# Kernel optimization log

Measured on AMD Instinct MI355X. Metric: run time of the kernel, lower is better.

The kernel has to match this reference:

```python
import jax, jax.numpy as jnp
import numpy as np


def _relu(x):
    return jnp.maximum(x, 0)


def _conv(x, w, b):
    # x: [M, Cin, H, W], w: [Cout, Cin, 3, 3], VALID padding, stride 1, ReLU
    y = jax.lax.conv_general_dilated(x, w, (1, 1), 'VALID',
                                     dimension_numbers=('NCHW', 'OIHW', 'NCHW'))
    return _relu(y + b[None, :, None, None])


def setup_inputs() -> dict:
    key = jax.random.key(0)
    ks = jax.random.split(key, 16)
    B, N, C, H, W = 32, 64, 16, 30, 30
    E, A = 128, 5
    s = 0.05
    f32 = jnp.float32
    states = jax.random.normal(ks[0], (B, N, C, H, W), f32)
    adjacencies = jax.random.uniform(ks[1], (B, N, N), f32)
    inactives = jax.random.randint(ks[2], (B, N), 0, 2).astype(bool)
    # conv block: C -> 16 -> 32 -> 16 -> 16, 3x3 VALID
    cw0 = jax.random.normal(ks[3], (16, C, 3, 3), f32) * s; cb0 = jnp.zeros((16,), f32)
    cw1 = jax.random.normal(ks[4], (32, 16, 3, 3), f32) * s; cb1 = jnp.zeros((32,), f32)
    cw2 = jax.random.normal(ks[5], (16, 32, 3, 3), f32) * s; cb2 = jnp.zeros((16,), f32)
    cw3 = jax.random.normal(ks[6], (16, 16, 3, 3), f32) * s; cb3 = jnp.zeros((16,), f32)
    flat = 16 * (H - 8) * (W - 8)  # 16*22*22 = 7744
    # encoder MLP: flat -> 128 -> 128 -> E
    mw0 = jax.random.normal(ks[7], (flat, 128), f32) * s; mb0 = jnp.zeros((128,), f32)
    mw1 = jax.random.normal(ks[8], (128, 128), f32) * s; mb1 = jnp.zeros((128,), f32)
    mw2 = jax.random.normal(ks[9], (128, E), f32) * s; mb2 = jnp.zeros((E,), f32)
    # GCNConv: E -> E
    gw = jax.random.normal(ks[10], (E, E), f32) * s; gb = jnp.zeros((E,), f32)
    # DQN head: E -> 128 -> 128 -> A
    fw0 = jax.random.normal(ks[11], (E, 128), f32) * s; fb0 = jnp.zeros((128,), f32)
    fw1 = jax.random.normal(ks[12], (128, 128), f32) * s; fb1 = jnp.zeros((128,), f32)
    fw2 = jax.random.normal(ks[13], (128, A), f32) * s; fb2 = jnp.zeros((A,), f32)
    return dict(states=states, adjacencies=adjacencies, inactives=inactives,
                cw0=cw0, cb0=cb0, cw1=cw1, cb1=cb1, cw2=cw2, cb2=cb2, cw3=cw3, cb3=cb3,
                mw0=mw0, mb0=mb0, mw1=mw1, mb1=mb1, mw2=mw2, mb2=mb2,
                gw=gw, gb=gb, fw0=fw0, fb0=fb0, fw1=fw1, fb1=fb1, fw2=fw2, fb2=fb2)


def reference(states, adjacencies, inactives,
              cw0, cb0, cw1, cb1, cw2, cb2, cw3, cb3,
              mw0, mb0, mw1, mb1, mw2, mb2,
              gw, gb, fw0, fb0, fw1, fb1, fw2, fb2):
    B, N = states.shape[0], states.shape[1]
    # per-agent CNN encoder, batched over all (batch, agent) pairs
    x = states.reshape((B * N,) + states.shape[2:])
    for w, b in ((cw0, cb0), (cw1, cb1), (cw2, cb2), (cw3, cb3)):
        x = _conv(x, w, b)
    x = x.reshape(B * N, -1)
    x = _relu(x @ mw0 + mb0)
    x = _relu(x @ mw1 + mb1)
    feats = (x @ mw2 + mb2).reshape(B, N, -1)  # [B, N, E]
    # GCNConv with symmetric normalization (add_self_loops=False; the original
    # edge-list loop is equivalent to dense propagation with A as edge weights)
    deg = adjacencies.sum(axis=1)  # deg[b, j] = sum_i A[b, i, j] (target degree)
    dis = jnp.where(deg > 0, jax.lax.rsqrt(jnp.maximum(deg, 1e-30)), 0.0)
    h = feats @ gw  # [B, N, E]
    norm = dis[:, :, None] * adjacencies * dis[:, None, :]  # norm[b, i, j]
    emb = jnp.einsum('bij,bid->bjd', norm, h) + gb  # messages i -> j
    # per-agent DQN head; inactive agents keep zero q-values
    q = _relu(emb @ fw0 + fb0)
    q = _relu(q @ fw1 + fb1)
    q = q @ fw2 + fb2  # [B, N, action_size]
    return jnp.where(inactives[..., None], 0.0, q)
```

## Files before the change

### kernel.cpp

```cpp
#include <hip/hip_runtime.h>


__global__ void k_mask(const void* __restrict__ raw, int* __restrict__ mask)
{
    __shared__ unsigned pat[8];
    __shared__ int layout;
    const unsigned char* bts = (const unsigned char*)raw;
    const unsigned* w = (const unsigned*)raw;
    const unsigned short* hw = (const unsigned short*)raw;
    const int t = threadIdx.x;
    if (t < 8) pat[t] = 0;
    __syncthreads();
    unsigned loc[8] = {0,0,0,0,0,0,0,0};
    for (int i = t * 8; i < 2048; i += 256 * 8)
#pragma unroll
        for (int r = 0; r < 8; ++r) loc[r] |= bts[i + r];
#pragma unroll
    for (int r = 0; r < 8; ++r) if (loc[r]) atomicOr(&pat[r], loc[r]);
    __syncthreads();
    if (t == 0) {
        int L = 0;
        bool smallOnly = true;
#pragma unroll
        for (int r = 0; r < 8; ++r) smallOnly = smallOnly && (pat[r] <= 1u);
        if (smallOnly) {
            if (pat[1] | pat[2] | pat[3] | pat[5] | pat[6] | pat[7]) L = 1;
            else if (pat[4] == 0 && pat[0])                          L = 2;
            else                                                     L = 0;
        } else {
            if (pat[1] | pat[5])      L = 4;
            else if (pat[2] | pat[6]) L = 3;
            else if (pat[7])          L = 5;
        }
        layout = L;
    }
    __syncthreads();
    const int L = layout;
    for (int m = t; m < 2048; m += 256) {
        unsigned v;
        if      (L == 1) v = bts[m];
        else if (L == 2) v = w[2 * m] | w[2 * m + 1];
        else if (L == 3) v = w[m];
        else if (L == 4) v = hw[m];
        else if (L == 5) v = w[2 * m] | w[2 * m + 1];
        else             v = w[m];
        mask[m] = (v != 0u);
    }
}

template<int OW>
__device__ __forceinline__ void row_sweep(
    const float* __restrict__ r0, const float* __restrict__ r1,
    const float* __restrict__ r2,
    const float* __restrict__ w0, const float* __restrict__ w1,
    float* __restrict__ acc0, float* __restrict__ acc1)
{
    float a[3][8] __attribute__((aligned(16)));
    *(float4*)&a[0][0] = *(const float4*)r0;
    *(float4*)&a[1][0] = *(const float4*)r1;
    *(float4*)&a[2][0] = *(const float4*)r2;
#pragma unroll
    for (int cx = 0; cx < OW; cx += 4) {
        if (OW - cx > 2) {
            *(float4*)&a[0][4] = *(const float4*)(r0 + cx + 4);
            *(float4*)&a[1][4] = *(const float4*)(r1 + cx + 4);
            *(float4*)&a[2][4] = *(const float4*)(r2 + cx + 4);
        }
#pragma unroll
        for (int j = 0; j < 4; ++j) {
            if (cx + j < OW) {
#pragma unroll
                for (int ky = 0; ky < 3; ++ky)
#pragma unroll
                    for (int kx = 0; kx < 3; ++kx) {
                        acc0[cx + j] = fmaf(w0[ky * 3 + kx], a[ky][j + kx], acc0[cx + j]);
                        acc1[cx + j] = fmaf(w1[ky * 3 + kx], a[ky][j + kx], acc1[cx + j]);
                    }
            }
        }
#pragma unroll
        for (int ky = 0; ky < 3; ++ky)
            *(float4*)&a[ky][0] = *(float4*)&a[ky][4];
    }
}

__global__ __launch_bounds__(256, 2)
void k_convA(const float* __restrict__ st,
             const float* __restrict__ cw0, const float* __restrict__ cb0,
             const float* __restrict__ cw1, const float* __restrict__ cb1,
             float* __restrict__ y1)
{
    __shared__ float sY0[16 * 784];
    __shared__ float sIn[2 * 1080];
    __shared__ float sW[2 * 384];
    const int t = threadIdx.x;
    const int bId = blockIdx.x;
    const float* stb = st + (size_t)bId * 14400;

    const int g0 = t >> 5;
    const int row0 = t & 31;
    const bool act0 = row0 < 28;

    float acc[2][28];
#pragma unroll
    for (int o = 0; o < 2; ++o)
#pragma unroll
        for (int c = 0; c < 28; ++c) acc[o][c] = 0.f;

    auto stage_in0 = [&](int ic, int buf) {
        if (t < 225) {
            float4 v = *(const float4*)&stb[ic * 900 + t * 4];
            float vv[4] = {v.x, v.y, v.z, v.w};
            int e = t * 4;
#pragma unroll
            for (int k = 0; k < 4; ++k) {
                int ee = e + k;
                sIn[buf * 1080 + (ee / 30) * 36 + (ee % 30)] = vv[k];
            }
        }
    };
    auto stage_w0 = [&](int ic, int buf) {
        if (t < 192) {
            int oc = t / 12, k = t % 12;
            if (k < 9) sW[buf * 384 + t] = cw0[(oc * 16 + ic) * 9 + k];
        }
    };

    stage_in0(0, 0); stage_w0(0, 0);
#pragma unroll 1
    for (int ic = 0; ic < 16; ++ic) {
        __syncthreads();
        if (ic + 1 < 16) { stage_in0(ic + 1, (ic + 1) & 1); stage_w0(ic + 1, (ic + 1) & 1); }
        if (act0) {
            const int buf = ic & 1;
            float w0r[12] __attribute__((aligned(16)));
            float w1r[12] __attribute__((aligned(16)));
#pragma unroll
            for (int q = 0; q < 3; ++q) {
                *(float4*)&w0r[q * 4] = *(const float4*)&sW[buf * 384 + (2 * g0 + 0) * 12 + q * 4];
                *(float4*)&w1r[q * 4] = *(const float4*)&sW[buf * 384 + (2 * g0 + 1) * 12 + q * 4];
            }
            const float* b = &sIn[buf * 1080 + row0 * 36];
            row_sweep<28>(b, b + 36, b + 72, w0r, w1r, acc[0], acc[1]);
        }
    }
    if (act0) {
#pragma unroll
        for (int o = 0; o < 2; ++o) {
            float bv = cb0[2 * g0 + o];
            float* dst = &sY0[(2 * g0 + o) * 784 + row0 * 28];
#pragma unroll
            for (int cx = 0; cx < 28; cx += 4) {
                float4 v;
                v.x = fmaxf(acc[o][cx + 0] + bv, 0.f);
                v.y = fmaxf(acc[o][cx + 1] + bv, 0.f);
                v.z = fmaxf(acc[o][cx + 2] + bv, 0.f);
                v.w = fmaxf(acc[o][cx + 3] + bv, 0.f);
                *(float4*)&dst[cx] = v;
            }
        }
    }
    __syncthreads();

    auto stage_w1 = [&](int ic, int buf) {
        for (int e = t; e < 384; e += 256) {
            int oc = e / 12, k = e % 12;
            if (k < 9) sW[buf * 384 + e] = cw1[(oc * 16 + ic) * 9 + k];
        }
    };
    stage_w1(0, 0);
    const int g1 = t >> 4;
    const int l1 = t & 15;
#pragma unroll 1
    for (int p = 0; p < 2; ++p) {
        const int row = l1 + 16 * p;
        const bool act1 = row < 26;
        float a1[2][26];
#pragma unroll
        for (int o = 0; o < 2; ++o)
#pragma unroll
            for (int c = 0; c < 26; ++c) a1[o][c] = 0.f;
#pragma unroll 1
        for (int ic = 0; ic < 16; ++ic) {
            __syncthreads();
            int s = p * 16 + ic;
            if (s + 1 < 32) stage_w1((s + 1) & 15, (s + 1) & 1);
            if (act1) {
                const int buf = s & 1;
                float w0r[12] __attribute__((aligned(16)));
                float w1r[12] __attribute__((aligned(16)));
#pragma unroll
                for (int q = 0; q < 3; ++q) {
                    *(float4*)&w0r[q * 4] = *(const float4*)&sW[buf * 384 + (2 * g1 + 0) * 12 + q * 4];
                    *(float4*)&w1r[q * 4] = *(const float4*)&sW[buf * 384 + (2 * g1 + 1) * 12 + q * 4];
                }
                const float* b = &sY0[ic * 784 + row * 28];
                row_sweep<26>(b, b + 28, b + 56, w0r, w1r, a1[0], a1[1]);
            }
        }
        if (act1) {
#pragma unroll
            for (int o = 0; o < 2; ++o) {
                float bv = cb1[2 * g1 + o];
                float* dst = &y1[((size_t)bId * 32 + (2 * g1 + o)) * 676 + row * 26];
#pragma unroll
                for (int cx = 0; cx < 26; cx += 2) {
                    float2 v;
                    v.x = fmaxf(a1[o][cx + 0] + bv, 0.f);
                    v.y = fmaxf(a1[o][cx + 1] + bv, 0.f);
                    *(float2*)&dst[cx] = v;
                }
            }
        }
    }
}

__global__ __launch_bounds__(256, 3)
void k_convB(const float* __restrict__ y1,
             const float* __restrict__ cw2, const float* __restrict__ cb2,
             const float* __restrict__ cw3, const float* __restrict__ cb3,
             float* __restrict__ y3)
{
    __shared__ float sY2[16 * 672];
    __shared__ float sIn[2 * 768];
    __shared__ float sW[2 * 192];
    const int t = threadIdx.x;
    const int bId = blockIdx.x;
    const int g = t >> 5;
    const int row = t & 31;

    const bool act2 = row < 24;
    float acc[2][24];
#pragma unroll
    for (int o = 0; o < 2; ++o)
#pragma unroll
        for (int c = 0; c < 24; ++c) acc[o][c] = 0.f;

    auto stage_in2 = [&](int ic, int buf) {
        if (t < 169) {
            float4 v = *(const float4*)&y1[((size_t)bId * 32 + ic) * 676 + t * 4];
            float vv[4] = {v.x, v.y, v.z, v.w};
            int e = t * 4;
#pragma unroll
            for (int k = 0; k < 4; ++k) {
                int ee = e + k;
                sIn[buf * 768 + (ee / 26) * 28 + (ee % 26)] = vv[k];
            }
        }
    };
    auto stage_w2 = [&](int ic, int buf) {
        if (t < 192) {
            int oc = t / 12, k = t % 12;
            if (k < 9) sW[buf * 192 + t] = cw2[(oc * 32 + ic) * 9 + k];
        }
    };

    stage_in2(0, 0); stage_w2(0, 0);
#pragma unroll 1
    for (int ic = 0; ic < 32; ++ic) {
        __syncthreads();
        if (ic + 1 < 32) { stage_in2(ic + 1, (ic + 1) & 1); stage_w2(ic + 1, (ic + 1) & 1); }
        if (act2) {
            const int buf = ic & 1;
            float w0r[12] __attribute__((aligned(16)));
            float w1r[12] __attribute__((aligned(16)));
#pragma unroll
            for (int q = 0; q < 3; ++q) {
                *(float4*)&w0r[q * 4] = *(const float4*)&sW[buf * 192 + (2 * g + 0) * 12 + q * 4];
                *(float4*)&w1r[q * 4] = *(const float4*)&sW[buf * 192 + (2 * g + 1) * 12 + q * 4];
            }
            const float* b = &sIn[buf * 768 + row * 28];
            row_sweep<24>(b, b + 28, b + 56, w0r, w1r, acc[0], acc[1]);
        }
    }
    if (act2) {
#pragma unroll
        for (int o = 0; o < 2; ++o) {
            float bv = cb2[2 * g + o];
            float* dst = &sY2[(2 * g + o) * 672 + row * 28];
#pragma unroll
            for (int cx = 0; cx < 24; cx += 4) {
                float4 v;
                v.x = fmaxf(acc[o][cx + 0] + bv, 0.f);
                v.y = fmaxf(acc[o][cx + 1] + bv, 0.f);
                v.z = fmaxf(acc[o][cx + 2] + bv, 0.f);
                v.w = fmaxf(acc[o][cx + 3] + bv, 0.f);
                *(float4*)&dst[cx] = v;
            }
        }
    }
    __syncthreads();

    auto stage_w3 = [&](int ic, int buf) {
        if (t < 192) {
            int oc = t / 12, k = t % 12;
            if (k < 9) sW[buf * 192 + t] = cw3[(oc * 16 + ic) * 9 + k];
        }
    };
    stage_w3(0, 0);
    const bool act3 = row < 22;
    float a3[2][22];
#pragma unroll
    for (int o = 0; o < 2; ++o)
#pragma unroll
        for (int c = 0; c < 22; ++c) a3[o][c] = 0.f;
#pragma unroll 1
    for (int ic = 0; ic < 16; ++ic) {
        __syncthreads();
        if (ic + 1 < 16) stage_w3(ic + 1, (ic + 1) & 1);
        if (act3) {
            const int buf = ic & 1;
            float w0r[12] __attribute__((aligned(16)));
            float w1r[12] __attribute__((aligned(16)));
#pragma unroll
            for (int q = 0; q < 3; ++q) {
                *(float4*)&w0r[q * 4] = *(const float4*)&sW[buf * 192 + (2 * g + 0) * 12 + q * 4];
                *(float4*)&w1r[q * 4] = *(const float4*)&sW[buf * 192 + (2 * g + 1) * 12 + q * 4];
            }
            const float* b = &sY2[ic * 672 + row * 28];
            row_sweep<22>(b, b + 28, b + 56, w0r, w1r, a3[0], a3[1]);
        }
    }
    if (act3) {
#pragma unroll
        for (int o = 0; o < 2; ++o) {
            float bv = cb3[2 * g + o];
            float* dst = &y3[(size_t)bId * 7744 + (2 * g + o) * 484 + row * 22];
#pragma unroll
            for (int cx = 0; cx < 22; cx += 2) {
                float2 v;
                v.x = fmaxf(a3[o][cx + 0] + bv, 0.f);
                v.y = fmaxf(a3[o][cx + 1] + bv, 0.f);
                *(float2*)&dst[cx] = v;
            }
        }
    }
}

__global__ __launch_bounds__(256)
void k_mlp0(const float* __restrict__ y3, const float* __restrict__ mw0,
            float* __restrict__ part)
{
    __shared__ float As[8 * 32];
    __shared__ float Bs[8 * 128];
    const int t  = threadIdx.x;
    const int mt = blockIdx.x;
    const int ks = blockIdx.y;
    const int m0g = mt * 32;
    const int kb0 = ks * 968;
    const int tm = t >> 4, tn = t & 15;
    const int m0 = tm * 2, n0 = tn * 8;
    float acc[2][8];
#pragma unroll
    for (int r = 0; r < 2; ++r)
#pragma unroll
        for (int c = 0; c < 8; ++c) acc[r][c] = 0.f;

    for (int it = 0; it < 121; ++it) {
        const int kb = kb0 + it * 8;
        if (t < 64) {
            int m = t >> 1, q = t & 1;
            const float4 a4 = *(const float4*)&y3[(m0g + m) * 7744 + kb + q * 4];
            As[(q * 4 + 0) * 32 + m] = a4.x;
            As[(q * 4 + 1) * 32 + m] = a4.y;
            As[(q * 4 + 2) * 32 + m] = a4.z;
            As[(q * 4 + 3) * 32 + m] = a4.w;
        }
        {
            int kk = t >> 5, n4 = t & 31;
            *(float4*)&Bs[kk * 128 + n4 * 4] = *(const float4*)&mw0[(kb + kk) * 128 + n4 * 4];
        }
        __syncthreads();
#pragma unroll
        for (int kk = 0; kk < 8; ++kk) {
            float a0 = As[kk * 32 + m0];
            float a1 = As[kk * 32 + m0 + 1];
            float4 b0 = *(const float4*)&Bs[kk * 128 + n0];
            float4 b1 = *(const float4*)&Bs[kk * 128 + n0 + 4];
            float br[8] = {b0.x, b0.y, b0.z, b0.w, b1.x, b1.y, b1.z, b1.w};
#pragma unroll
            for (int c = 0; c < 8; ++c) {
                acc[0][c] = fmaf(a0, br[c], acc[0][c]);
                acc[1][c] = fmaf(a1, br[c], acc[1][c]);
            }
        }
        __syncthreads();
    }
#pragma unroll
    for (int r = 0; r < 2; ++r)
#pragma unroll
        for (int c = 0; c < 8; ++c)
            part[ks * 262144 + (m0g + m0 + r) * 128 + n0 + c] = acc[r][c];
}

__global__ void k_red(const float* __restrict__ part, const float* __restrict__ mb0,
                      float* __restrict__ z0)
{
    int idx = blockIdx.x * 256 + threadIdx.x;
    int n = idx & 127;
    float s = mb0[n];
#pragma unroll
    for (int k = 0; k < 8; ++k) s += part[k * 262144 + idx];
    z0[idx] = fmaxf(s, 0.f);
}

__global__ __launch_bounds__(256)
void k_fc(const float* __restrict__ A, const float* __restrict__ W,
          const float* __restrict__ bias, float* __restrict__ C, int do_relu)
{
    __shared__ float As[32 * 129];
    __shared__ float Ws[32 * 128];
    const int t = threadIdx.x;
    const int m0g = blockIdx.x * 32;
#pragma unroll
    for (int r = 0; r < 16; ++r) {
        int e = t + r * 256; int m = e >> 7, k = e & 127;
        As[m * 129 + k] = A[(m0g + m) * 128 + k];
    }
    const int tm = t >> 4, tn = t & 15;
    const int m0 = tm * 2, n0 = tn * 8;
    float acc[2][8];
#pragma unroll
    for (int r = 0; r < 2; ++r)
#pragma unroll
        for (int c = 0; c < 8; ++c) acc[r][c] = 0.f;

    for (int kc = 0; kc < 4; ++kc) {
        __syncthreads();
#pragma unroll
        for (int r = 0; r < 16; ++r) {
            int e = t + r * 256; int kk = e >> 7, n = e & 127;
            Ws[kk * 128 + n] = W[(kc * 32 + kk) * 128 + n];
        }
        __syncthreads();
#pragma unroll
        for (int kk = 0; kk < 32; ++kk) {
            float a0 = As[(m0 + 0) * 129 + kc * 32 + kk];
            float a1 = As[(m0 + 1) * 129 + kc * 32 + kk];
            float4 b0 = *(const float4*)&Ws[kk * 128 + n0];
            float4 b1 = *(const float4*)&Ws[kk * 128 + n0 + 4];
            float br[8] = {b0.x, b0.y, b0.z, b0.w, b1.x, b1.y, b1.z, b1.w};
#pragma unroll
            for (int c = 0; c < 8; ++c) {
                acc[0][c] = fmaf(a0, br[c], acc[0][c]);
                acc[1][c] = fmaf(a1, br[c], acc[1][c]);
            }
        }
    }
#pragma unroll
    for (int c = 0; c < 8; ++c) {
        float bv = bias ? bias[n0 + c] : 0.f;
#pragma unroll
        for (int r = 0; r < 2; ++r) {
            float v = acc[r][c] + bv;
            if (do_relu) v = fmaxf(v, 0.f);
            C[(m0g + m0 + r) * 128 + n0 + c] = v;
        }
    }
}

__global__ void k_dis(const float* __restrict__ adj, float* __restrict__ dis)
{
    int bj = blockIdx.x * 256 + threadIdx.x;
    int b = bj >> 6, j = bj & 63;
    float s = 0.f;
#pragma unroll 4
    for (int i = 0; i < 64; ++i) s += adj[b * 4096 + i * 64 + j];
    dis[bj] = s > 0.f ? rsqrtf(fmaxf(s, 1e-30f)) : 0.f;
}

__global__ __launch_bounds__(256)
void k_gcn(const float* __restrict__ adj, const float* __restrict__ dis,
           const float* __restrict__ h, const float* __restrict__ gb,
           float* __restrict__ emb)
{
    __shared__ float adjn[64 * 64];
    __shared__ float hS[64 * 128];
    __shared__ float disS[64];
    const int t = threadIdx.x;
    const int b = blockIdx.x;
    if (t < 64) disS[t] = dis[b * 64 + t];
    __syncthreads();
#pragma unroll
    for (int r = 0; r < 16; ++r) {
        int e = t + r * 256; int i = e >> 6;
        adjn[e] = adj[b * 4096 + e] * disS[i];
    }
#pragma unroll
    for (int r = 0; r < 32; ++r) {
        int e = t + r * 256;
        hS[e] = h[b * 8192 + e];
    }
    __syncthreads();
    const int tj = t >> 5, tn = t & 31;
    const int j0 = tj * 8, n0 = tn * 4;
    float acc[8][4];
#pragma unroll
    for (int jj = 0; jj < 8; ++jj)
#pragma unroll
        for (int c = 0; c < 4; ++c) acc[jj][c] = 0.f;
    for (int i = 0; i < 64; ++i) {
        float4 h4 = *(const float4*)&hS[i * 128 + n0];
        float hr[4] = {h4.x, h4.y, h4.z, h4.w};
#pragma unroll
        for (int jj = 0; jj < 8; ++jj) {
            float a = adjn[i * 64 + j0 + jj];
#pragma unroll
            for (int c = 0; c < 4; ++c) acc[jj][c] = fmaf(a, hr[c], acc[jj][c]);
        }
    }
#pragma unroll
    for (int jj = 0; jj < 8; ++jj) {
        float dj = disS[j0 + jj];
#pragma unroll
        for (int c = 0; c < 4; ++c)
            emb[b * 8192 + (j0 + jj) * 128 + n0 + c] = dj * acc[jj][c] + gb[n0 + c];
    }
}

__global__ __launch_bounds__(256)
void k_head(const float* __restrict__ q1, const float* __restrict__ fw2,
            const float* __restrict__ fb2, const int* __restrict__ maskN,
            float* __restrict__ out)
{
    __shared__ float qs[256 * 33];
    __shared__ float w2s[640];
    __shared__ float b2s[5];
    const int t = threadIdx.x;
    const int m0g = blockIdx.x * 256;
    if (t < 5) b2s[t] = fb2[t];
#pragma unroll
    for (int r = 0; r < 3; ++r) {
        int e = t + r * 256;
        if (e < 640) w2s[e] = fw2[e];
    }
    float acc[5] = {0.f, 0.f, 0.f, 0.f, 0.f};
    for (int kc = 0; kc < 4; ++kc) {
        __syncthreads();
#pragma unroll
        for (int r = 0; r < 32; ++r) {
            int e = t + r * 256; int m = e >> 5, k = e & 31;
            qs[m * 33 + k] = q1[(m0g + m) * 128 + kc * 32 + k];
        }
        __syncthreads();
#pragma unroll
        for (int k = 0; k < 32; ++k) {
            float v = qs[t * 33 + k];
#pragma unroll
            for (int a = 0; a < 5; ++a) acc[a] = fmaf(v, w2s[(kc * 32 + k) * 5 + a], acc[a]);
        }
    }
    const int m = m0g + t;
    const int iz = maskN[m];
#pragma unroll
    for (int a = 0; a < 5; ++a) out[m * 5 + a] = iz ? 0.f : (acc[a] + b2s[a]);
}

extern "C" void kernel_launch(void* const* d_in, const int* in_sizes, int n_in,
                              void* d_out, int out_size, void* d_ws, size_t ws_size,
                              hipStream_t stream)
{
    (void)in_sizes; (void)n_in; (void)out_size;
    const float* states = (const float*)d_in[0];
    const float* adj    = (const float*)d_in[1];
    const void*  inact  = (const void*) d_in[2];
    const float* cw0 = (const float*)d_in[3];  const float* cb0 = (const float*)d_in[4];
    const float* cw1 = (const float*)d_in[5];  const float* cb1 = (const float*)d_in[6];
    const float* cw2 = (const float*)d_in[7];  const float* cb2 = (const float*)d_in[8];
    const float* cw3 = (const float*)d_in[9];  const float* cb3 = (const float*)d_in[10];
    const float* mw0 = (const float*)d_in[11]; const float* mb0 = (const float*)d_in[12];
    const float* mw1 = (const float*)d_in[13]; const float* mb1 = (const float*)d_in[14];
    const float* mw2 = (const float*)d_in[15]; const float* mb2 = (const float*)d_in[16];
    const float* gw  = (const float*)d_in[17]; const float* gb  = (const float*)d_in[18];
    const float* fw0 = (const float*)d_in[19]; const float* fb0 = (const float*)d_in[20];
    const float* fw1 = (const float*)d_in[21]; const float* fb1 = (const float*)d_in[22];
    const float* fw2 = (const float*)d_in[23]; const float* fb2 = (const float*)d_in[24];
    float* out = (float*)d_out;

    const size_t HDR_FL = 4096, Y3_FL = 15859712, TAIL_FL = 3932160;
    const size_t Y1_PER_IMG = 21632;
    size_t ws_fl = ws_size / 4;
    int nsplit = 32;
    for (int n = 1; n <= 32; n *= 2) {
        size_t imgs = (2048 + (size_t)n - 1) / n;
        size_t y1fl = imgs * Y1_PER_IMG;
        size_t need = HDR_FL + Y3_FL + (y1fl > TAIL_FL ? y1fl : TAIL_FL);
        if (need <= ws_fl) { nsplit = n; break; }
    }

    float* ws    = (float*)d_ws;
    int*   maskN = (int*)ws;
    float* dis   = ws + 2048;
    float* y3    = ws + HDR_FL;
    float* dyn   = y3 + Y3_FL;
    float* y1g   = dyn;
    float* part  = dyn;
    float* z0    = part + 2097152;
    float* z1    = z0   + 262144;
    float* feats = z1   + 262144;
    float* h     = feats + 262144;
    float* emb   = h    + 262144;
    float* q0    = emb  + 262144;
    float* q1    = q0   + 262144;

    k_mask<<<1, 256, 0, stream>>>(inact, maskN);

    const int per = (2048 + nsplit - 1) / nsplit;
    for (int s = 0; s < nsplit; ++s) {
        int i0 = s * per;
        int cnt = 2048 - i0; if (cnt > per) cnt = per;
        if (cnt <= 0) break;
        k_convA<<<cnt, 256, 0, stream>>>(states + (size_t)i0 * 14400,
                                         cw0, cb0, cw1, cb1, y1g);
        k_convB<<<cnt, 256, 0, stream>>>(y1g, cw2, cb2, cw3, cb3,
                                         y3 + (size_t)i0 * 7744);
    }

    k_mlp0<<<dim3(64, 8), 256, 0, stream>>>(y3, mw0, part);
    k_red<<<1024, 256, 0, stream>>>(part, mb0, z0);
    k_fc<<<64, 256, 0, stream>>>(z0, mw1, mb1, z1, 1);
    k_fc<<<64, 256, 0, stream>>>(z1, mw2, mb2, feats, 0);
    k_fc<<<64, 256, 0, stream>>>(feats, gw, nullptr, h, 0);
    k_dis<<<8, 256, 0, stream>>>(adj, dis);
    k_gcn<<<32, 256, 0, stream>>>(adj, dis, h, gb, emb);
    k_fc<<<64, 256, 0, stream>>>(emb, fw0, fb0, q0, 1);
    k_fc<<<64, 256, 0, stream>>>(q0, fw1, fb1, q1, 1);
    k_head<<<8, 256, 0, stream>>>(q1, fw2, fb2, maskN, out);
}
```

Measured before the change: 1.033 ms.

## Preload conv weights into shared memory once and enlarge mlp0 tile

The conv kernels now stage each layer's full weight set into shared memory once, in an arena that reuses the input staging buffers. This removes per-input-channel weight staging and most barriers in the conv1 and conv3 loops. The first MLP GEMM tile grows from 32 to 64 rows per block, with a 4x8 register tile per thread and split column groups, so each weight tile is reused across more rows. Shared memory grows and the mlp0 grid halves, which may reduce occupancy or parallelism.

```diff
diff --git a/kernel.cpp b/kernel.cpp
--- a/kernel.cpp
+++ b/kernel.cpp
@@ -90,12 +90,22 @@
              const float* __restrict__ cw1, const float* __restrict__ cb1,
              float* __restrict__ y1)
 {
-    __shared__ float sY0[16 * 784];
-    __shared__ float sIn[2 * 1080];
-    __shared__ float sW[2 * 384];
+    __shared__ float arena[12544 + 6272];
+    float* const sY0 = arena;
+    float* const regB = arena + 12544;
+    float* const sIn = regB;
+    float* const sW0 = regB + 2160;
+    float* const sW1 = regB;
+
     const int t = threadIdx.x;
     const int bId = blockIdx.x;
     const float* stb = st + (size_t)bId * 14400;
+
+    {
+#pragma unroll
+        for (int k = 0; k < 9; ++k)
+            sW0[(t >> 4) * 196 + (t & 15) * 12 + k] = cw0[t * 9 + k];
+    }
 
     const int g0 = t >> 5;
     const int row0 = t & 31;
@@ -119,26 +129,20 @@
             }
         }
     };
-    auto stage_w0 = [&](int ic, int buf) {
-        if (t < 192) {
-            int oc = t / 12, k = t % 12;
-            if (k < 9) sW[buf * 384 + t] = cw0[(oc * 16 + ic) * 9 + k];
-        }
-    };
-
-    stage_in0(0, 0); stage_w0(0, 0);
+
+    stage_in0(0, 0);
 #pragma unroll 1
     for (int ic = 0; ic < 16; ++ic) {
         __syncthreads();
-        if (ic + 1 < 16) { stage_in0(ic + 1, (ic + 1) & 1); stage_w0(ic + 1, (ic + 1) & 1); }
+        if (ic + 1 < 16) stage_in0(ic + 1, (ic + 1) & 1);
         if (act0) {
             const int buf = ic & 1;
             float w0r[12] __attribute__((aligned(16)));
             float w1r[12] __attribute__((aligned(16)));
 #pragma unroll
             for (int q = 0; q < 3; ++q) {
-                *(float4*)&w0r[q * 4] = *(const float4*)&sW[buf * 384 + (2 * g0 + 0) * 12 + q * 4];
-                *(float4*)&w1r[q * 4] = *(const float4*)&sW[buf * 384 + (2 * g0 + 1) * 12 + q * 4];
+                *(float4*)&w0r[q * 4] = *(const float4*)&sW0[(2 * g0 + 0) * 196 + ic * 12 + q * 4];
+                *(float4*)&w1r[q * 4] = *(const float4*)&sW0[(2 * g0 + 1) * 196 + ic * 12 + q * 4];
             }
             const float* b = &sIn[buf * 1080 + row0 * 36];
             row_sweep<28>(b, b + 36, b + 72, w0r, w1r, acc[0], acc[1]);
@@ -162,13 +166,14 @@
     }
     __syncthreads();
 
-    auto stage_w1 = [&](int ic, int buf) {
-        for (int e = t; e < 384; e += 256) {
-            int oc = e / 12, k = e % 12;
-            if (k < 9) sW[buf * 384 + e] = cw1[(oc * 16 + ic) * 9 + k];
-        }
-    };
-    stage_w1(0, 0);
+    for (int e = t; e < 512; e += 256) {
+        int oc = e >> 4, ic = e & 15;
+#pragma unroll
+        for (int k = 0; k < 9; ++k)
+            sW1[oc * 196 + ic * 12 + k] = cw1[e * 9 + k];
+    }
+    __syncthreads();
+
     const int g1 = t >> 4;
     const int l1 = t & 15;
 #pragma unroll 1
@@ -180,25 +185,19 @@
         for (int o = 0; o < 2; ++o)
 #pragma unroll
             for (int c = 0; c < 26; ++c) a1[o][c] = 0.f;
+        if (act1) {
 #pragma unroll 1
-        for (int ic = 0; ic < 16; ++ic) {
-            __syncthreads();
-            int s = p * 16 + ic;
-            if (s + 1 < 32) stage_w1((s + 1) & 15, (s + 1) & 1);
-            if (act1) {
-                const int buf = s & 1;
+            for (int ic = 0; ic < 16; ++ic) {
                 float w0r[12] __attribute__((aligned(16)));
                 float w1r[12] __attribute__((aligned(16)));
 #pragma unroll
                 for (int q = 0; q < 3; ++q) {
-                    *(float4*)&w0r[q * 4] = *(const float4*)&sW[buf * 384 + (2 * g1 + 0) * 12 + q * 4];
-                    *(float4*)&w1r[q * 4] = *(const float4*)&sW[buf * 384 + (2 * g1 + 1) * 12 + q * 4];
+                    *(float4*)&w0r[q * 4] = *(const float4*)&sW1[(2 * g1 + 0) * 196 + ic * 12 + q * 4];
+                    *(float4*)&w1r[q * 4] = *(const float4*)&sW1[(2 * g1 + 1) * 196 + ic * 12 + q * 4];
                 }
                 const float* b = &sY0[ic * 784 + row * 28];
                 row_sweep<26>(b, b + 28, b + 56, w0r, w1r, a1[0], a1[1]);
             }
-        }
-        if (act1) {
 #pragma unroll
             for (int o = 0; o < 2; ++o) {
                 float bv = cb1[2 * g1 + o];
@@ -221,9 +220,13 @@
              const float* __restrict__ cw3, const float* __restrict__ cb3,
              float* __restrict__ y3)
 {
-    __shared__ float sY2[16 * 672];
-    __shared__ float sIn[2 * 768];
-    __shared__ float sW[2 * 192];
+    __shared__ float arena2[10752 + 2304];
+    float* const sY2 = arena2;
+    float* const regB = arena2 + 10752;
+    float* const sIn = regB;
+    float* const sW2 = regB + 1536;
+    float* const sW3 = regB;
+
     const int t = threadIdx.x;
     const int bId = blockIdx.x;
     const int g = t >> 5;
@@ -251,7 +254,7 @@
     auto stage_w2 = [&](int ic, int buf) {
         if (t < 192) {
             int oc = t / 12, k = t % 12;
-            if (k < 9) sW[buf * 192 + t] = cw2[(oc * 32 + ic) * 9 + k];
+            if (k < 9) sW2[buf * 192 + t] = cw2[(oc * 32 + ic) * 9 + k];
         }
     };
 
@@ -266,8 +269,8 @@
             float w1r[12] __attribute__((aligned(16)));
 #pragma unroll
             for (int q = 0; q < 3; ++q) {
-                *(float4*)&w0r[q * 4] = *(const float4*)&sW[buf * 192 + (2 * g + 0) * 12 + q * 4];
-                *(float4*)&w1r[q * 4] = *(const float4*)&sW[buf * 192 + (2 * g + 1) * 12 + q * 4];
+                *(float4*)&w0r[q * 4] = *(const float4*)&sW2[buf * 192 + (2 * g + 0) * 12 + q * 4];
+                *(float4*)&w1r[q * 4] = *(const float4*)&sW2[buf * 192 + (2 * g + 1) * 12 + q * 4];
             }
             const float* b = &sIn[buf * 768 + row * 28];
             row_sweep<24>(b, b + 28, b + 56, w0r, w1r, acc[0], acc[1]);
@@ -291,37 +294,27 @@
     }
     __syncthreads();
 
-    auto stage_w3 = [&](int ic, int buf) {
-        if (t < 192) {
-            int oc = t / 12, k = t % 12;
-            if (k < 9) sW[buf * 192 + t] = cw3[(oc * 16 + ic) * 9 + k];
-        }
-    };
-    stage_w3(0, 0);
+    for (int e = t; e < 2304; e += 256) sW3[e] = cw3[e];
+    __syncthreads();
+
     const bool act3 = row < 22;
     float a3[2][22];
 #pragma unroll
     for (int o = 0; o < 2; ++o)
 #pragma unroll
         for (int c = 0; c < 22; ++c) a3[o][c] = 0.f;
+    if (act3) {
 #pragma unroll 1
-    for (int ic = 0; ic < 16; ++ic) {
-        __syncthreads();
-        if (ic + 1 < 16) stage_w3(ic + 1, (ic + 1) & 1);
-        if (act3) {
-            const int buf = ic & 1;
-            float w0r[12] __attribute__((aligned(16)));
-            float w1r[12] __attribute__((aligned(16)));
-#pragma unroll
-            for (int q = 0; q < 3; ++q) {
-                *(float4*)&w0r[q * 4] = *(const float4*)&sW[buf * 192 + (2 * g + 0) * 12 + q * 4];
-                *(float4*)&w1r[q * 4] = *(const float4*)&sW[buf * 192 + (2 * g + 1) * 12 + q * 4];
+        for (int ic = 0; ic < 16; ++ic) {
+            float w0r[9], w1r[9];
+#pragma unroll
+            for (int k = 0; k < 9; ++k) {
+                w0r[k] = sW3[((2 * g + 0) * 16 + ic) * 9 + k];
+                w1r[k] = sW3[((2 * g + 1) * 16 + ic) * 9 + k];
             }
             const float* b = &sY2[ic * 672 + row * 28];
             row_sweep<22>(b, b + 28, b + 56, w0r, w1r, a3[0], a3[1]);
         }
-    }
-    if (act3) {
 #pragma unroll
         for (int o = 0; o < 2; ++o) {
             float bv = cb3[2 * g + o];
@@ -341,30 +334,30 @@
 void k_mlp0(const float* __restrict__ y3, const float* __restrict__ mw0,
             float* __restrict__ part)
 {
-    __shared__ float As[8 * 32];
+    __shared__ float As[8 * 64];
     __shared__ float Bs[8 * 128];
     const int t  = threadIdx.x;
     const int mt = blockIdx.x;
     const int ks = blockIdx.y;
-    const int m0g = mt * 32;
+    const int m0g = mt * 64;
     const int kb0 = ks * 968;
     const int tm = t >> 4, tn = t & 15;
-    const int m0 = tm * 2, n0 = tn * 8;
-    float acc[2][8];
-#pragma unroll
-    for (int r = 0; r < 2; ++r)
+    const int m0 = tm * 4, n0 = tn * 4;
+    float acc[4][8];
+#pragma unroll
+    for (int r = 0; r < 4; ++r)
 #pragma unroll
         for (int c = 0; c < 8; ++c) acc[r][c] = 0.f;
 
     for (int it = 0; it < 121; ++it) {
         const int kb = kb0 + it * 8;
-        if (t < 64) {
+        if (t < 128) {
             int m = t >> 1, q = t & 1;
             const float4 a4 = *(const float4*)&y3[(m0g + m) * 7744 + kb + q * 4];
-            As[(q * 4 + 0) * 32 + m] = a4.x;
-            As[(q * 4 + 1) * 32 + m] = a4.y;
-            As[(q * 4 + 2) * 32 + m] = a4.z;
-            As[(q * 4 + 3) * 32 + m] = a4.w;
+            As[(q * 4 + 0) * 64 + m] = a4.x;
+            As[(q * 4 + 1) * 64 + m] = a4.y;
+            As[(q * 4 + 2) * 64 + m] = a4.z;
+            As[(q * 4 + 3) * 64 + m] = a4.w;
         }
         {
             int kk = t >> 5, n4 = t & 31;
@@ -373,24 +366,27 @@
         __syncthreads();
 #pragma unroll
         for (int kk = 0; kk < 8; ++kk) {
-            float a0 = As[kk * 32 + m0];
-            float a1 = As[kk * 32 + m0 + 1];
+            float ar[4];
+#pragma unroll
+            for (int r = 0; r < 4; ++r) ar[r] = As[kk * 64 + m0 + r];
             float4 b0 = *(const float4*)&Bs[kk * 128 + n0];
-            float4 b1 = *(const float4*)&Bs[kk * 128 + n0 + 4];
+            float4 b1 = *(const float4*)&Bs[kk * 128 + 64 + n0];
             float br[8] = {b0.x, b0.y, b0.z, b0.w, b1.x, b1.y, b1.z, b1.w};
 #pragma unroll
-            for (int c = 0; c < 8; ++c) {
-                acc[0][c] = fmaf(a0, br[c], acc[0][c]);
-                acc[1][c] = fmaf(a1, br[c], acc[1][c]);
-            }
-        }
-        __syncthreads();
-    }
-#pragma unroll
-    for (int r = 0; r < 2; ++r)
-#pragma unroll
-        for (int c = 0; c < 8; ++c)
-            part[ks * 262144 + (m0g + m0 + r) * 128 + n0 + c] = acc[r][c];
+            for (int r = 0; r < 4; ++r)
+#pragma unroll
+                for (int c = 0; c < 8; ++c)
+                    acc[r][c] = fmaf(ar[r], br[c], acc[r][c]);
+        }
+        __syncthreads();
+    }
+#pragma unroll
+    for (int r = 0; r < 4; ++r)
+#pragma unroll
+        for (int c = 0; c < 8; ++c) {
+            int col = (c < 4) ? (n0 + c) : (64 + n0 + c - 4);
+            part[ks * 262144 + (m0g + m0 + r) * 128 + col] = acc[r][c];
+        }
 }
 
 __global__ void k_red(const float* __restrict__ part, const float* __restrict__ mb0,
@@ -616,7 +612,7 @@
                                          y3 + (size_t)i0 * 7744);
     }
 
-    k_mlp0<<<dim3(64, 8), 256, 0, stream>>>(y3, mw0, part);
+    k_mlp0<<<dim3(32, 8), 256, 0, stream>>>(y3, mw0, part);
     k_red<<<1024, 256, 0, stream>>>(part, mb0, z0);
     k_fc<<<64, 256, 0, stream>>>(z0, mw1, mb1, z1, 1);
     k_fc<<<64, 256, 0, stream>>>(z1, mw2, mb2, feats, 0);
```

New measurement: 987.0 us. -4.5%, faster.
